# Optimization experiments

Hardware: AMD Instinct MI355X
Metric: run time of the kernel (lower is better)

The kernel has to match this reference:

```python
import jax, jax.numpy as jnp
import numpy as np

B, N, D, K = 1024, 8192, 256, 8
LAMBDA_MULT = 0.01

def setup_inputs() -> dict:
    key = jax.random.key(0)
    k1, k2, k3, k4, k5 = jax.random.split(key, 5)
    x = jax.random.uniform(k1, (B, D), dtype=jnp.float32)
    mu = jax.random.uniform(k2, (N, D), dtype=jnp.float32)
    lambda_base = jax.random.uniform(k3, (N,), dtype=jnp.float32) * LAMBDA_MULT
    v = jax.random.normal(k4, (N, K, D), dtype=jnp.float32)  # stands in for per-unit orthogonal init
    omega = 0.1 + 0.4 * jax.random.uniform(k5, (N, K), dtype=jnp.float32)
    return {"x": x, "mu": mu, "lambda_base": lambda_base, "v": v, "omega": omega}

def reference(x, mu, lambda_base, v, omega):
    # quad_form = diff^T (lambda*I + sum_k omega_k v_k v_k^T) diff
    #           = lambda * ||x - mu||^2 + sum_k omega_k * ((x - mu) . v_k)^2
    # Woodbury-style expansion avoids materializing W:(n,d,d) and diff:(b,n,d).
    x2 = jnp.sum(x * x, axis=-1)                      # (b,)
    mu2 = jnp.sum(mu * mu, axis=-1)                   # (n,)
    xm = x @ mu.T                                     # (b,n)
    sqdist = x2[:, None] - 2.0 * xm + mu2[None, :]    # (b,n) = ||x-mu||^2
    xv = jnp.einsum('bd,nkd->bnk', x, v)              # (b,n,k)
    muv = jnp.einsum('nd,nkd->nk', mu, v)             # (n,k)
    proj2 = (xv - muv[None, :, :]) ** 2               # (b,n,k)
    quad = lambda_base[None, :] * sqdist + jnp.einsum('bnk,nk->bn', proj2, omega)
    return jnp.exp(-quad / D)  # Type == 'exp'
```

## Files before the change

### kernel.cpp

```cpp
#include <hip/hip_runtime.h>


#define B_SZ 1024
#define N_SZ 8192
#define D_SZ 256
#define K_SZ 8

#define BT 128
#define NT 16

typedef __bf16 bf16x8 __attribute__((ext_vector_type(8)));
typedef float f32x4 __attribute__((ext_vector_type(4)));
typedef unsigned short u16x4 __attribute__((ext_vector_type(4)));
typedef unsigned short u16x8 __attribute__((ext_vector_type(8)));

#define WS_X2   0u
#define WS_MU2  4096u
#define WS_MUV  36864u
#define WS_PX   299008u
#define WS_PW   823296u
#define WS_NEED (823296ull + 37748736ull)

__device__ __forceinline__ float wave_reduce(float s) {
#pragma unroll
  for (int off = 32; off > 0; off >>= 1) s += __shfl_down(s, off);
  return s;
}

__device__ __forceinline__ u16x4 cvt4(float4 t) {
  u16x4 r;
  r[0] = __builtin_bit_cast(unsigned short, (__bf16)t.x);
  r[1] = __builtin_bit_cast(unsigned short, (__bf16)t.y);
  r[2] = __builtin_bit_cast(unsigned short, (__bf16)t.z);
  r[3] = __builtin_bit_cast(unsigned short, (__bf16)t.w);
  return r;
}

__device__ __forceinline__ void glds16(const void* g, const void* l) {
  __builtin_amdgcn_global_load_lds(
      (const __attribute__((address_space(1))) void*)g,
      (__attribute__((address_space(3))) void*)l, 16, 0, 0);
}

__global__ void prep_x(const float* __restrict__ x, float* __restrict__ x2,
                       unsigned short* __restrict__ px) {
  const int w = threadIdx.x >> 6, lane = threadIdx.x & 63;
  const int b = blockIdx.x * 4 + w;
  float4 t = *(const float4*)(x + (size_t)b * D_SZ + 4 * lane);
  *(u16x4*)(px + (size_t)b * D_SZ + 4 * lane) = cvt4(t);
  float s = t.x * t.x + t.y * t.y + t.z * t.z + t.w * t.w;
  s = wave_reduce(s);
  if (lane == 0) x2[b] = s;
}

__global__ void prep_w(const float* __restrict__ mu, const float* __restrict__ v,
                       float* __restrict__ mu2, float* __restrict__ muv,
                       unsigned short* __restrict__ pw) {
  __shared__ __align__(16) float mulds[D_SZ];
  const int n = blockIdx.x;
  const int w = threadIdx.x >> 6, lane = threadIdx.x & 63;
  if (w == 0) {
    float4 m4 = *(const float4*)(mu + (size_t)n * D_SZ + 4 * lane);
    *(float4*)(mulds + 4 * lane) = m4;
    *(u16x4*)(pw + (size_t)n * 9 * D_SZ + 4 * lane) = cvt4(m4);
    float s = m4.x * m4.x + m4.y * m4.y + m4.z * m4.z + m4.w * m4.w;
    s = wave_reduce(s);
    if (lane == 0) mu2[n] = s;
  }
  __syncthreads();
  float4 m4 = *(const float4*)(mulds + 4 * lane);
#pragma unroll
  for (int kk = 0; kk < 2; ++kk) {
    const int k = w * 2 + kk;
    float4 v4 = *(const float4*)(v + ((size_t)n * K_SZ + k) * D_SZ + 4 * lane);
    *(u16x4*)(pw + ((size_t)n * 9 + k + 1) * D_SZ + 4 * lane) = cvt4(v4);
    float s = m4.x * v4.x + m4.y * v4.y + m4.z * v4.z + m4.w * v4.w;
    s = wave_reduce(s);
    if (lane == 0) muv[n * K_SZ + k] = s;
  }
}

__global__ __launch_bounds__(256, 2)
void hmu_main_p(const unsigned short* __restrict__ px,
                const unsigned short* __restrict__ pw,
                const float* __restrict__ lam, const float* __restrict__ om,
                const float* __restrict__ wsf, float* __restrict__ out) {
  __shared__ __align__(16) unsigned short As[BT * 32];
  __shared__ __align__(16) unsigned short Bs[NT * 9 * 32];

  const float* ws_x2 = wsf;
  const float* ws_mu2 = wsf + 1024;
  const float* ws_muv = wsf + 9216;

  const int tid = threadIdx.x;
  const int lane = tid & 63;
  const int w = tid >> 6;
  const int m = lane & 15;
  const int kg = lane >> 4;
  const int nl4 = lane >> 2;
  const int ch = lane & 3;

  const int n0 = blockIdx.x * NT;
  const int b0 = blockIdx.y * BT;

  f32x4 acc[2][9];
#pragma unroll
  for (int bs = 0; bs < 2; ++bs)
#pragma unroll
    for (int j = 0; j < 9; ++j) acc[bs][j] = (f32x4){0.f, 0.f, 0.f, 0.f};

  for (int kt = 0; kt < 8; ++kt) {
    const int k0 = kt * 32;
#pragma unroll
    for (int t = 0; t < 2; ++t) {
      int r0 = w * 32 + t * 16;
      glds16(px + (size_t)(b0 + r0 + nl4) * D_SZ + k0 + ch * 8, As + r0 * 32);
    }
#pragma unroll
    for (int t = 0; t < 3; ++t) {
      int i = w + 4 * t;
      if (i < 9)
        glds16(pw + ((size_t)(n0 + nl4) * 9 + i) * D_SZ + k0 + ch * 8,
               Bs + i * 16 * 32);
    }
    __syncthreads();

    bf16x8 af[2];
#pragma unroll
    for (int bs = 0; bs < 2; ++bs)
      af[bs] = *(const bf16x8*)&As[((2 * w + bs) * 16 + m) * 32 + kg * 8];
#pragma unroll
    for (int j = 0; j < 9; ++j) {
      bf16x8 bfr = *(const bf16x8*)&Bs[(j * 16 + m) * 32 + kg * 8];
      acc[0][j] = __builtin_amdgcn_mfma_f32_16x16x32_bf16(af[0], bfr, acc[0][j], 0, 0, 0);
      acc[1][j] = __builtin_amdgcn_mfma_f32_16x16x32_bf16(af[1], bfr, acc[1][j], 0, 0, 0);
    }
    __syncthreads();
  }

  const int n = n0 + m;
  const float lam_n = lam[n];
  const float mu2_n = ws_mu2[n];
  float omr[8], muvr[8];
#pragma unroll
  for (int k = 0; k < 8; ++k) {
    omr[k] = om[n * 8 + k];
    muvr[k] = ws_muv[n * 8 + k];
  }
#pragma unroll
  for (int bs = 0; bs < 2; ++bs) {
#pragma unroll
    for (int r = 0; r < 4; ++r) {
      int b = b0 + (2 * w + bs) * 16 + kg * 4 + r;
      float x2b = ws_x2[b];
      float c0 = acc[bs][0][r];
      float q = lam_n * (x2b - 2.f * c0 + mu2_n);
#pragma unroll
      for (int k = 0; k < 8; ++k) {
        float p = acc[bs][k + 1][r] - muvr[k];
        q = fmaf(omr[k] * p, p, q);
      }
      out[(size_t)b * N_SZ + n] = __expf(q * (-1.0f / 256.0f));
    }
  }
}

__device__ __forceinline__ void cvt16_store(const float* __restrict__ src,
                                            unsigned short* dst) {
  const float4* p4 = (const float4*)src;
  float fv[16];
#pragma unroll
  for (int e = 0; e < 4; ++e) {
    float4 t = p4[e];
    fv[4 * e + 0] = t.x; fv[4 * e + 1] = t.y;
    fv[4 * e + 2] = t.z; fv[4 * e + 3] = t.w;
  }
  u16x8 lo, hi;
#pragma unroll
  for (int e = 0; e < 8; ++e) {
    lo[e] = __builtin_bit_cast(unsigned short, (__bf16)fv[e]);
    hi[e] = __builtin_bit_cast(unsigned short, (__bf16)fv[e + 8]);
  }
  *(u16x8*)dst = lo;
  *(u16x8*)(dst + 8) = hi;
}

#define LDS_STRIDE 40
__global__ __launch_bounds__(256, 2)
void hmu_main_f(const float* __restrict__ x, const float* __restrict__ mu,
                const float* __restrict__ lam, const float* __restrict__ v,
                const float* __restrict__ om, const float* __restrict__ ws,
                float* __restrict__ out) {
  __shared__ __align__(16) unsigned short As[BT * LDS_STRIDE];
  __shared__ __align__(16) unsigned short Bs[NT * 9 * LDS_STRIDE];
  const float* ws_x2 = ws;
  const float* ws_mu2 = ws + 1024;
  const float* ws_muv = ws + 9216;
  const int tid = threadIdx.x, lane = tid & 63, w = tid >> 6;
  const int m = lane & 15, kg = lane >> 4;
  const int n0 = blockIdx.x * NT, b0 = blockIdx.y * BT;
  f32x4 acc[2][9];
#pragma unroll
  for (int bs = 0; bs < 2; ++bs)
#pragma unroll
    for (int j = 0; j < 9; ++j) acc[bs][j] = (f32x4){0.f, 0.f, 0.f, 0.f};
  const int arow = tid >> 1, ahalf = tid & 1;
  for (int kt = 0; kt < 8; ++kt) {
    const int k0 = kt * 32;
    cvt16_store(x + (size_t)(b0 + arow) * D_SZ + k0 + ahalf * 16,
                &As[arow * LDS_STRIDE + ahalf * 16]);
#pragma unroll
    for (int it = 0; it < 2; ++it) {
      int idx = tid + 256 * it;
      if (idx < 288) {
        int row = idx >> 1, half = idx & 1;
        int nl = row / 9, j = row - nl * 9;
        const float* src = (j == 0)
            ? mu + (size_t)(n0 + nl) * D_SZ + k0 + half * 16
            : v + (size_t)((n0 + nl) * K_SZ + (j - 1)) * D_SZ + k0 + half * 16;
        cvt16_store(src, &Bs[row * LDS_STRIDE + half * 16]);
      }
    }
    __syncthreads();
    bf16x8 af[2];
#pragma unroll
    for (int bs = 0; bs < 2; ++bs)
      af[bs] = *(const bf16x8*)&As[((2 * w + bs) * 16 + m) * LDS_STRIDE + kg * 8];
#pragma unroll
    for (int j = 0; j < 9; ++j) {
      bf16x8 bfr = *(const bf16x8*)&Bs[(m * 9 + j) * LDS_STRIDE + kg * 8];
      acc[0][j] = __builtin_amdgcn_mfma_f32_16x16x32_bf16(af[0], bfr, acc[0][j], 0, 0, 0);
      acc[1][j] = __builtin_amdgcn_mfma_f32_16x16x32_bf16(af[1], bfr, acc[1][j], 0, 0, 0);
    }
    __syncthreads();
  }
  const int n = n0 + m;
  const float lam_n = lam[n];
  const float mu2_n = ws_mu2[n];
  float omr[8], muvr[8];
#pragma unroll
  for (int k = 0; k < 8; ++k) {
    omr[k] = om[n * 8 + k];
    muvr[k] = ws_muv[n * 8 + k];
  }
#pragma unroll
  for (int bs = 0; bs < 2; ++bs)
#pragma unroll
    for (int r = 0; r < 4; ++r) {
      int b = b0 + (2 * w + bs) * 16 + kg * 4 + r;
      float c0 = acc[bs][0][r];
      float q = lam_n * (ws_x2[b] - 2.f * c0 + mu2_n);
#pragma unroll
      for (int k = 0; k < 8; ++k) {
        float p = acc[bs][k + 1][r] - muvr[k];
        q = fmaf(omr[k] * p, p, q);
      }
      out[(size_t)b * N_SZ + n] = __expf(q * (-1.0f / 256.0f));
    }
}

__global__ void p2_mu_f(const float* __restrict__ mu, const float* __restrict__ v,
                        float* __restrict__ mu2, float* __restrict__ muv) {
  __shared__ __align__(16) float mulds[D_SZ];
  const int n = blockIdx.x;
  const int w = threadIdx.x >> 6, lane = threadIdx.x & 63;
  if (w == 0) {
    float4 m4 = *(const float4*)(mu + (size_t)n * D_SZ + 4 * lane);
    *(float4*)(mulds + 4 * lane) = m4;
    float s = m4.x * m4.x + m4.y * m4.y + m4.z * m4.z + m4.w * m4.w;
    s = wave_reduce(s);
    if (lane == 0) mu2[n] = s;
  }
  __syncthreads();
  float4 m4 = *(const float4*)(mulds + 4 * lane);
#pragma unroll
  for (int kk = 0; kk < 2; ++kk) {
    const int k = w * 2 + kk;
    float4 v4 = *(const float4*)(v + ((size_t)n * K_SZ + k) * D_SZ + 4 * lane);
    float s = m4.x * v4.x + m4.y * v4.y + m4.z * v4.z + m4.w * v4.w;
    s = wave_reduce(s);
    if (lane == 0) muv[n * K_SZ + k] = s;
  }
}

__global__ void p1_x2_f(const float* __restrict__ x, float* __restrict__ x2) {
  const int w = threadIdx.x >> 6, lane = threadIdx.x & 63;
  const int b = blockIdx.x * 4 + w;
  float4 t = *(const float4*)(x + (size_t)b * D_SZ + 4 * lane);
  float s = t.x * t.x + t.y * t.y + t.z * t.z + t.w * t.w;
  s = wave_reduce(s);
  if (lane == 0) x2[b] = s;
}

extern "C" void kernel_launch(void* const* d_in, const int* in_sizes, int n_in,
                              void* d_out, int out_size, void* d_ws, size_t ws_size,
                              hipStream_t stream) {
  const float* x   = (const float*)d_in[0];
  const float* mu  = (const float*)d_in[1];
  const float* lam = (const float*)d_in[2];
  const float* v   = (const float*)d_in[3];
  const float* om  = (const float*)d_in[4];
  float* out = (float*)d_out;
  char* wsb = (char*)d_ws;
  float* wsf = (float*)d_ws;
  float* x2  = (float*)(wsb + WS_X2);
  float* mu2 = (float*)(wsb + WS_MU2);
  float* muv = (float*)(wsb + WS_MUV);

  dim3 grid(N_SZ / NT, B_SZ / BT);
  if (ws_size >= WS_NEED) {
    unsigned short* px = (unsigned short*)(wsb + WS_PX);
    unsigned short* pw = (unsigned short*)(wsb + WS_PW);
    prep_x<<<B_SZ / 4, 256, 0, stream>>>(x, x2, px);
    prep_w<<<N_SZ, 256, 0, stream>>>(mu, v, mu2, muv, pw);
    hmu_main_p<<<grid, 256, 0, stream>>>(px, pw, lam, om, wsf, out);
  } else {
    p1_x2_f<<<B_SZ / 4, 256, 0, stream>>>(x, x2);
    p2_mu_f<<<N_SZ, 256, 0, stream>>>(mu, v, mu2, muv);
    hmu_main_f<<<grid, 256, 0, stream>>>(x, mu, lam, v, om, wsf, out);
  }
}
```

Measured before the change: 170.9 us.

## Fuse weight prep into main kernel and keep N-tile resident across all B tiles

Drops the separate prep_w kernel and its 37MB bf16 workspace round trip. Each block now converts its 16 mu/v rows to bf16 straight into LDS and computes mu2 and muv there. It then loops over all 8 batch tiles, reusing the resident B operand and reading x fragments directly from global/L2 without LDS staging. This cuts global traffic and a kernel launch. The cost is only 512 blocks, more LDS per block (about 78KB), and unstaged A loads that may stall the MFMA loop.

```diff
diff --git a/kernel.cpp b/kernel.cpp
--- a/kernel.cpp
+++ b/kernel.cpp
@@ -6,20 +6,21 @@
 #define D_SZ 256
 #define K_SZ 8
 
+#define NT 16
 #define BT 128
-#define NT 16
+#define NBT (B_SZ / BT)
 
 typedef __bf16 bf16x8 __attribute__((ext_vector_type(8)));
 typedef float f32x4 __attribute__((ext_vector_type(4)));
 typedef unsigned short u16x4 __attribute__((ext_vector_type(4)));
 typedef unsigned short u16x8 __attribute__((ext_vector_type(8)));
 
-#define WS_X2   0u
-#define WS_MU2  4096u
-#define WS_MUV  36864u
-#define WS_PX   299008u
-#define WS_PW   823296u
-#define WS_NEED (823296ull + 37748736ull)
+#define WS_X2 0u
+#define WS_PX 4096u
+#define WS_NEED_P (4096ull + 524288ull)
+#define WS_MU2F 4096u
+#define WS_MUVF 36864u
+#define WS_NEED_F 299008ull
 
 __device__ __forceinline__ float wave_reduce(float s) {
 #pragma unroll
@@ -34,12 +35,6 @@
   r[2] = __builtin_bit_cast(unsigned short, (__bf16)t.z);
   r[3] = __builtin_bit_cast(unsigned short, (__bf16)t.w);
   return r;
-}
-
-__device__ __forceinline__ void glds16(const void* g, const void* l) {
-  __builtin_amdgcn_global_load_lds(
-      (const __attribute__((address_space(1))) void*)g,
-      (__attribute__((address_space(3))) void*)l, 16, 0, 0);
 }
 
 __global__ void prep_x(const float* __restrict__ x, float* __restrict__ x2,
@@ -53,115 +48,100 @@
   if (lane == 0) x2[b] = s;
 }
 
-__global__ void prep_w(const float* __restrict__ mu, const float* __restrict__ v,
-                       float* __restrict__ mu2, float* __restrict__ muv,
-                       unsigned short* __restrict__ pw) {
-  __shared__ __align__(16) float mulds[D_SZ];
-  const int n = blockIdx.x;
-  const int w = threadIdx.x >> 6, lane = threadIdx.x & 63;
-  if (w == 0) {
-    float4 m4 = *(const float4*)(mu + (size_t)n * D_SZ + 4 * lane);
-    *(float4*)(mulds + 4 * lane) = m4;
-    *(u16x4*)(pw + (size_t)n * 9 * D_SZ + 4 * lane) = cvt4(m4);
-    float s = m4.x * m4.x + m4.y * m4.y + m4.z * m4.z + m4.w * m4.w;
-    s = wave_reduce(s);
-    if (lane == 0) mu2[n] = s;
-  }
-  __syncthreads();
-  float4 m4 = *(const float4*)(mulds + 4 * lane);
-#pragma unroll
-  for (int kk = 0; kk < 2; ++kk) {
-    const int k = w * 2 + kk;
-    float4 v4 = *(const float4*)(v + ((size_t)n * K_SZ + k) * D_SZ + 4 * lane);
-    *(u16x4*)(pw + ((size_t)n * 9 + k + 1) * D_SZ + 4 * lane) = cvt4(v4);
-    float s = m4.x * v4.x + m4.y * v4.y + m4.z * v4.z + m4.w * v4.w;
-    s = wave_reduce(s);
-    if (lane == 0) muv[n * K_SZ + k] = s;
-  }
-}
-
 __global__ __launch_bounds__(256, 2)
-void hmu_main_p(const unsigned short* __restrict__ px,
-                const unsigned short* __restrict__ pw,
-                const float* __restrict__ lam, const float* __restrict__ om,
-                const float* __restrict__ wsf, float* __restrict__ out) {
-  __shared__ __align__(16) unsigned short As[BT * 32];
-  __shared__ __align__(16) unsigned short Bs[NT * 9 * 32];
-
-  const float* ws_x2 = wsf;
-  const float* ws_mu2 = wsf + 1024;
-  const float* ws_muv = wsf + 9216;
+void hmu_pers(const unsigned short* __restrict__ px,
+              const float* __restrict__ mu, const float* __restrict__ v,
+              const float* __restrict__ lam, const float* __restrict__ om,
+              const float* __restrict__ x2g, float* __restrict__ out) {
+  __shared__ __align__(16) unsigned short Bs[8 * 144 * 32];
+  __shared__ __align__(16) float x2s[B_SZ];
+  __shared__ float mu2s[NT];
+  __shared__ float muvs[NT * K_SZ];
 
   const int tid = threadIdx.x;
   const int lane = tid & 63;
   const int w = tid >> 6;
-  const int m = lane & 15;
-  const int kg = lane >> 4;
-  const int nl4 = lane >> 2;
-  const int ch = lane & 3;
-
   const int n0 = blockIdx.x * NT;
-  const int b0 = blockIdx.y * BT;
-
-  f32x4 acc[2][9];
-#pragma unroll
-  for (int bs = 0; bs < 2; ++bs)
-#pragma unroll
-    for (int j = 0; j < 9; ++j) acc[bs][j] = (f32x4){0.f, 0.f, 0.f, 0.f};
-
-  for (int kt = 0; kt < 8; ++kt) {
-    const int k0 = kt * 32;
-#pragma unroll
-    for (int t = 0; t < 2; ++t) {
-      int r0 = w * 32 + t * 16;
-      glds16(px + (size_t)(b0 + r0 + nl4) * D_SZ + k0 + ch * 8, As + r0 * 32);
-    }
-#pragma unroll
-    for (int t = 0; t < 3; ++t) {
-      int i = w + 4 * t;
-      if (i < 9)
-        glds16(pw + ((size_t)(n0 + nl4) * 9 + i) * D_SZ + k0 + ch * 8,
-               Bs + i * 16 * 32);
-    }
-    __syncthreads();
-
-    bf16x8 af[2];
-#pragma unroll
-    for (int bs = 0; bs < 2; ++bs)
-      af[bs] = *(const bf16x8*)&As[((2 * w + bs) * 16 + m) * 32 + kg * 8];
-#pragma unroll
-    for (int j = 0; j < 9; ++j) {
-      bf16x8 bfr = *(const bf16x8*)&Bs[(j * 16 + m) * 32 + kg * 8];
-      acc[0][j] = __builtin_amdgcn_mfma_f32_16x16x32_bf16(af[0], bfr, acc[0][j], 0, 0, 0);
-      acc[1][j] = __builtin_amdgcn_mfma_f32_16x16x32_bf16(af[1], bfr, acc[1][j], 0, 0, 0);
-    }
-    __syncthreads();
-  }
-
+
+  *(float4*)(x2s + 4 * tid) = *(const float4*)(x2g + 4 * tid);
+
+  const int kts = lane >> 3;
+  const int c4 = (lane & 7) * 4;
+#pragma unroll 1
+  for (int nn = 0; nn < 4; ++nn) {
+    const int nl = w * 4 + nn;
+    const int n = n0 + nl;
+    float4 m4 = *(const float4*)(mu + (size_t)n * D_SZ + 4 * lane);
+    *(u16x4*)&Bs[kts * 4608 + nl * 32 + c4] = cvt4(m4);
+    float s2 = m4.x * m4.x + m4.y * m4.y + m4.z * m4.z + m4.w * m4.w;
+    float dk[K_SZ];
+#pragma unroll
+    for (int k = 0; k < K_SZ; ++k) {
+      float4 v4 = *(const float4*)(v + ((size_t)n * K_SZ + k) * D_SZ + 4 * lane);
+      *(u16x4*)&Bs[kts * 4608 + ((k + 1) * NT + nl) * 32 + c4] = cvt4(v4);
+      dk[k] = m4.x * v4.x + m4.y * v4.y + m4.z * v4.z + m4.w * v4.w;
+    }
+    s2 = wave_reduce(s2);
+    if (lane == 0) mu2s[nl] = s2;
+#pragma unroll
+    for (int k = 0; k < K_SZ; ++k) {
+      float r = wave_reduce(dk[k]);
+      if (lane == 0) muvs[nl * K_SZ + k] = r;
+    }
+  }
+  __syncthreads();
+
+  const int m = lane & 15, kg = lane >> 4;
   const int n = n0 + m;
   const float lam_n = lam[n];
-  const float mu2_n = ws_mu2[n];
-  float omr[8], muvr[8];
-#pragma unroll
-  for (int k = 0; k < 8; ++k) {
-    omr[k] = om[n * 8 + k];
-    muvr[k] = ws_muv[n * 8 + k];
-  }
-#pragma unroll
-  for (int bs = 0; bs < 2; ++bs) {
-#pragma unroll
-    for (int r = 0; r < 4; ++r) {
-      int b = b0 + (2 * w + bs) * 16 + kg * 4 + r;
-      float x2b = ws_x2[b];
-      float c0 = acc[bs][0][r];
-      float q = lam_n * (x2b - 2.f * c0 + mu2_n);
-#pragma unroll
-      for (int k = 0; k < 8; ++k) {
-        float p = acc[bs][k + 1][r] - muvr[k];
-        q = fmaf(omr[k] * p, p, q);
+  const float mu2_n = mu2s[m];
+  float omr[K_SZ], muvr[K_SZ];
+#pragma unroll
+  for (int k = 0; k < K_SZ; ++k) {
+    omr[k] = om[n * K_SZ + k];
+    muvr[k] = muvs[m * K_SZ + k];
+  }
+
+  const unsigned short* pxw = px + (size_t)(w * 32 + m) * D_SZ + kg * 8;
+
+  for (int bt = 0; bt < NBT; ++bt) {
+    const int brow = bt * BT + w * 32;
+    f32x4 acc[2][9];
+#pragma unroll
+    for (int rb = 0; rb < 2; ++rb)
+#pragma unroll
+      for (int j = 0; j < 9; ++j) acc[rb][j] = (f32x4){0.f, 0.f, 0.f, 0.f};
+
+#pragma unroll
+    for (int kt = 0; kt < 8; ++kt) {
+      bf16x8 bfr[9];
+#pragma unroll
+      for (int j = 0; j < 9; ++j)
+        bfr[j] = *(const bf16x8*)&Bs[kt * 4608 + (j * NT + m) * 32 + kg * 8];
+#pragma unroll
+      for (int rb = 0; rb < 2; ++rb) {
+        bf16x8 a = *(const bf16x8*)(pxw + ((size_t)bt * BT + rb * 16) * D_SZ + kt * 32);
+#pragma unroll
+        for (int j = 0; j < 9; ++j)
+          acc[rb][j] = __builtin_amdgcn_mfma_f32_16x16x32_bf16(a, bfr[j], acc[rb][j], 0, 0, 0);
       }
-      out[(size_t)b * N_SZ + n] = __expf(q * (-1.0f / 256.0f));
-    }
+    }
+
+#pragma unroll
+    for (int rb = 0; rb < 2; ++rb)
+#pragma unroll
+      for (int r = 0; r < 4; ++r) {
+        int b = brow + rb * 16 + kg * 4 + r;
+        float x2b = x2s[b];
+        float c0 = acc[rb][0][r];
+        float q = lam_n * (x2b - 2.f * c0 + mu2_n);
+#pragma unroll
+        for (int k = 0; k < K_SZ; ++k) {
+          float p = acc[rb][k + 1][r] - muvr[k];
+          q = fmaf(omr[k] * p, p, q);
+        }
+        out[(size_t)b * N_SZ + n] = __expf(q * (-1.0f / 256.0f));
+      }
   }
 }
 
@@ -302,19 +282,18 @@
   const float* om  = (const float*)d_in[4];
   float* out = (float*)d_out;
   char* wsb = (char*)d_ws;
-  float* wsf = (float*)d_ws;
-  float* x2  = (float*)(wsb + WS_X2);
-  float* mu2 = (float*)(wsb + WS_MU2);
-  float* muv = (float*)(wsb + WS_MUV);
-
-  dim3 grid(N_SZ / NT, B_SZ / BT);
-  if (ws_size >= WS_NEED) {
+
+  if (ws_size >= WS_NEED_P) {
+    float* x2 = (float*)(wsb + WS_X2);
     unsigned short* px = (unsigned short*)(wsb + WS_PX);
-    unsigned short* pw = (unsigned short*)(wsb + WS_PW);
     prep_x<<<B_SZ / 4, 256, 0, stream>>>(x, x2, px);
-    prep_w<<<N_SZ, 256, 0, stream>>>(mu, v, mu2, muv, pw);
-    hmu_main_p<<<grid, 256, 0, stream>>>(px, pw, lam, om, wsf, out);
+    hmu_pers<<<N_SZ / NT, 256, 0, stream>>>(px, mu, v, lam, om, x2, out);
   } else {
+    float* wsf = (float*)d_ws;
+    float* x2  = (float*)(wsb + WS_X2);
+    float* mu2 = (float*)(wsb + WS_MU2F);
+    float* muv = (float*)(wsb + WS_MUVF);
+    dim3 grid(N_SZ / NT, B_SZ / BT);
     p1_x2_f<<<B_SZ / 4, 256, 0, stream>>>(x, x2);
     p2_mu_f<<<N_SZ, 256, 0, stream>>>(mu, v, mu2, muv);
     hmu_main_f<<<grid, 256, 0, stream>>>(x, mu, lam, v, om, wsf, out);
```

Result: slower. 256.9 us (+50.3%).
